# Kernel optimization log

Measured on AMD Instinct MI355X. Metric: run time of the kernel, lower is better.

The kernel has to match this reference:

```python
import jax, jax.numpy as jnp
import numpy as np

TEMPERATURE = 0.07
MARGIN = 0.15
HARD_NEG_RATIO = 0.5


def setup_inputs() -> dict:
    key = jax.random.key(0)
    k1, k2, k3 = jax.random.split(key, 3)
    B, D = 4096, 128
    drug_emb = jax.random.normal(k1, (B, D), dtype=jnp.float32)
    se_emb = jax.random.normal(k2, (B, D), dtype=jnp.float32)
    # labels spread over [0, 5) so that |diff| > 1.0 negatives exist
    labels = jax.random.uniform(k3, (B,), dtype=jnp.float32) * 5.0
    return {"drug_emb": drug_emb, "se_emb": se_emb, "labels": labels}


def _single_branch_loss(z, labels):
    B = z.shape[0]
    # F.normalize(z, dim=-1): divide by norm clamped to eps
    z = z / jnp.maximum(jnp.linalg.norm(z, axis=-1, keepdims=True), 1e-12)
    sim = jnp.matmul(z, z.T) / TEMPERATURE                      # [B, B]
    label_diff = jnp.abs(labels[None, :] - labels[:, None])     # [B, B]
    self_mask = ~jnp.eye(B, dtype=bool)
    pos_weight = jnp.exp(-label_diff / MARGIN) * self_mask      # soft positives
    neg_mask = (label_diff > 1.0) & self_mask

    # k = max(int(mean per-row negative count * ratio), 1), capped at B-1
    mean_negs = jnp.mean(jnp.sum(neg_mask.astype(jnp.float32), axis=1))
    k = jnp.maximum((mean_negs * HARD_NEG_RATIO).astype(jnp.int32), 1)
    k = jnp.minimum(k, B - 1)

    sim_max = jax.lax.stop_gradient(jnp.max(sim, axis=1, keepdims=True))
    logits = sim - sim_max

    # hard-negative top-k per row, as a static-shape rank test (jit-safe)
    neg_sim = jnp.where(neg_mask, sim, -jnp.inf)
    ranks = jnp.argsort(jnp.argsort(-neg_sim, axis=1), axis=1)  # 0 = largest
    hard_neg_mask = (ranks < k) & neg_mask

    any_neg = jnp.any(neg_mask)
    denom_mask = jnp.where(any_neg, hard_neg_mask | (pos_weight > 0.1), self_mask)

    exp_denom = jnp.sum(jnp.exp(logits) * denom_mask, axis=1, keepdims=True) + 1e-8
    log_prob = logits - jnp.log(exp_denom)
    weighted_log_prob = jnp.sum(pos_weight * log_prob, axis=1)
    denom = jnp.maximum(jnp.sum(pos_weight, axis=1), 1e-8)
    return -jnp.mean(weighted_log_prob / denom)


def reference(drug_emb, se_emb, labels):
    loss_drug = _single_branch_loss(drug_emb, labels)
    loss_se = _single_branch_loss(se_emb, labels)
    loss_cross = _single_branch_loss(drug_emb * se_emb, labels)
    return (loss_drug + loss_se + loss_cross) / 3.0
```

## Files before the change

kernel.cpp:

```cpp
#include <hip/hip_runtime.h>
#include <math.h>

#define BB 4096
#define DD 128
#define KLO 0x3E7FFFFFu
#define KHI 0xC1800000u
#define SH0 19
#define NBALLOC 4352

typedef __attribute__((ext_vector_type(8))) short bf16x8;
typedef __attribute__((ext_vector_type(4))) float f32x4;

__device__ __forceinline__ unsigned fkey(float x){
    int b = __float_as_int(x);
    return (unsigned)(b ^ ((b >> 31) | 0x80000000));
}
__device__ __forceinline__ float funkey(unsigned u){
    unsigned b = (u & 0x80000000u) ? (u & 0x7fffffffu) : ~u;
    return __uint_as_float(b);
}

__device__ __forceinline__ float blkSumF(float v, volatile float* sh){
    #pragma unroll
    for (int o = 32; o > 0; o >>= 1) v += __shfl_down(v, o);
    int t = threadIdx.x;
    __syncthreads();
    if ((t & 63) == 0) sh[t >> 6] = v;
    __syncthreads();
    return (sh[0] + sh[1]) + (sh[2] + sh[3]);
}
__device__ __forceinline__ int blkSumI(int v, volatile int* sh){
    #pragma unroll
    for (int o = 32; o > 0; o >>= 1) v += __shfl_down(v, o);
    int t = threadIdx.x;
    __syncthreads();
    if ((t & 63) == 0) sh[t >> 6] = v;
    __syncthreads();
    return (sh[0] + sh[1]) + (sh[2] + sh[3]);
}

__global__ void krn_normalize(const float* __restrict__ drug, const float* __restrict__ se,
                              const float* __restrict__ labels,
                              ushort* __restrict__ Z,
                              float* __restrict__ wp, float* __restrict__ wm){
    int row = blockIdx.x, br = blockIdx.y, t = threadIdx.x;
    float dv = drug[row * DD + t];
    float sv = se[row * DD + t];
    float v = (br == 0) ? dv : ((br == 1) ? sv : dv * sv);
    float sq = v * v;
    #pragma unroll
    for (int o = 32; o > 0; o >>= 1) sq += __shfl_down(sq, o);
    __shared__ float sh[2];
    if ((t & 63) == 0) sh[t >> 6] = sq;
    __syncthreads();
    float nrm = sqrtf(sh[0] + sh[1]);
    float outv = v / fmaxf(nrm, 1e-12f);
    unsigned u = __float_as_uint(outv);
    unsigned r = (u + 0x7FFFu + ((u >> 16) & 1u)) >> 16;
    int col = t ^ ((row & 7) << 3);
    Z[((size_t)br * BB + row) * DD + col] = (ushort)r;
    if (br == 0 && t == 0){
        float l = labels[row];
        wp[row] = __expf(l * (1.0f / 0.15f));
        wm[row] = __expf(l * (-1.0f / 0.15f));
    }
}

__global__ __launch_bounds__(256) void krn_negcount(const float* __restrict__ labels,
                                                    int* __restrict__ ntot){
    __shared__ float lab[BB];
    __shared__ int shi[4];
    int t = threadIdx.x;
    #pragma unroll
    for (int e = 0; e < 4; ++e)
        ((float4*)lab)[t + e * 256] = ((const float4*)labels)[t + e * 256];
    __syncthreads();
    int i0 = blockIdx.x * 16;
    int c = 0;
    for (int ii = 0; ii < 16; ++ii){
        float li = lab[i0 + ii];
        #pragma unroll
        for (int e = 0; e < 16; ++e){
            int j = t + e * 256;
            c += (fabsf(li - lab[j]) > 1.0f) ? 1 : 0;
        }
    }
    int cc = blkSumI(c, shi);
    if (t == 0) atomicAdd(ntot, cc);
}

__global__ void krn_calck(const int* __restrict__ ntot, int* __restrict__ kflags){
    int N = *ntot;
    int k = N >> 13;
    if (k < 1) k = 1;
    if (k > BB - 1) k = BB - 1;
    kflags[0] = k;
    kflags[1] = (N > 0) ? 1 : 0;
}

__device__ __forceinline__ bf16x8 frag_ld(const ushort* base, int row, int e0){
    int e = e0 ^ ((row & 7) << 3);
    return *(const bf16x8*)(base + row * DD + e);
}

__global__ __launch_bounds__(256) void krn_gemm(const ushort* __restrict__ Z,
                                                float* __restrict__ sim, size_t simStride,
                                                int r0){
    __shared__ ushort As[128 * DD];
    __shared__ ushort Bs[128 * DD];
    const ushort* Zb = Z + (size_t)blockIdx.z * (BB * DD);
    float* simz = sim + (size_t)blockIdx.z * simStride;
    int t = threadIdx.x;
    int rowbase = r0 + blockIdx.y * 128;
    int colbase = blockIdx.x * 128;

    {
        const float4* gA = (const float4*)(Zb + (size_t)rowbase * DD);
        const float4* gB = (const float4*)(Zb + (size_t)colbase * DD);
        float4* lA = (float4*)As;
        float4* lB = (float4*)Bs;
        #pragma unroll
        for (int it = 0; it < 8; ++it){
            lA[it * 256 + t] = gA[it * 256 + t];
            lB[it * 256 + t] = gB[it * 256 + t];
        }
    }
    __syncthreads();

    int wid = t >> 6, lane = t & 63;
    int wr = (wid >> 1) * 64, wc = (wid & 1) * 64;
    int fr = lane & 15, fq = lane >> 4;

    f32x4 acc[4][4];
    #pragma unroll
    for (int m = 0; m < 4; ++m)
        #pragma unroll
        for (int n = 0; n < 4; ++n)
            acc[m][n] = (f32x4){0.f, 0.f, 0.f, 0.f};

    #pragma unroll
    for (int ks = 0; ks < 4; ++ks){
        int e0 = ks * 32 + fq * 8;
        bf16x8 a0 = frag_ld(As, wr + 0 * 16 + fr, e0);
        bf16x8 a1 = frag_ld(As, wr + 1 * 16 + fr, e0);
        bf16x8 a2 = frag_ld(As, wr + 2 * 16 + fr, e0);
        bf16x8 a3 = frag_ld(As, wr + 3 * 16 + fr, e0);
        bf16x8 b0 = frag_ld(Bs, wc + 0 * 16 + fr, e0);
        bf16x8 b1 = frag_ld(Bs, wc + 1 * 16 + fr, e0);
        bf16x8 b2 = frag_ld(Bs, wc + 2 * 16 + fr, e0);
        bf16x8 b3 = frag_ld(Bs, wc + 3 * 16 + fr, e0);
        acc[0][0] = __builtin_amdgcn_mfma_f32_16x16x32_bf16(a0, b0, acc[0][0], 0, 0, 0);
        acc[0][1] = __builtin_amdgcn_mfma_f32_16x16x32_bf16(a0, b1, acc[0][1], 0, 0, 0);
        acc[0][2] = __builtin_amdgcn_mfma_f32_16x16x32_bf16(a0, b2, acc[0][2], 0, 0, 0);
        acc[0][3] = __builtin_amdgcn_mfma_f32_16x16x32_bf16(a0, b3, acc[0][3], 0, 0, 0);
        acc[1][0] = __builtin_amdgcn_mfma_f32_16x16x32_bf16(a1, b0, acc[1][0], 0, 0, 0);
        acc[1][1] = __builtin_amdgcn_mfma_f32_16x16x32_bf16(a1, b1, acc[1][1], 0, 0, 0);
        acc[1][2] = __builtin_amdgcn_mfma_f32_16x16x32_bf16(a1, b2, acc[1][2], 0, 0, 0);
        acc[1][3] = __builtin_amdgcn_mfma_f32_16x16x32_bf16(a1, b3, acc[1][3], 0, 0, 0);
        acc[2][0] = __builtin_amdgcn_mfma_f32_16x16x32_bf16(a2, b0, acc[2][0], 0, 0, 0);
        acc[2][1] = __builtin_amdgcn_mfma_f32_16x16x32_bf16(a2, b1, acc[2][1], 0, 0, 0);
        acc[2][2] = __builtin_amdgcn_mfma_f32_16x16x32_bf16(a2, b2, acc[2][2], 0, 0, 0);
        acc[2][3] = __builtin_amdgcn_mfma_f32_16x16x32_bf16(a2, b3, acc[2][3], 0, 0, 0);
        acc[3][0] = __builtin_amdgcn_mfma_f32_16x16x32_bf16(a3, b0, acc[3][0], 0, 0, 0);
        acc[3][1] = __builtin_amdgcn_mfma_f32_16x16x32_bf16(a3, b1, acc[3][1], 0, 0, 0);
        acc[3][2] = __builtin_amdgcn_mfma_f32_16x16x32_bf16(a3, b2, acc[3][2], 0, 0, 0);
        acc[3][3] = __builtin_amdgcn_mfma_f32_16x16x32_bf16(a3, b3, acc[3][3], 0, 0, 0);
    }

    const float invT = 1.0f / 0.07f;
    int srow0 = blockIdx.y * 128 + wr + fq * 4;
    int scol0 = colbase + wc + fr;
    #pragma unroll
    for (int m = 0; m < 4; ++m){
        #pragma unroll
        for (int n = 0; n < 4; ++n){
            f32x4 c = acc[m][n];
            #pragma unroll
            for (int j = 0; j < 4; ++j)
                simz[(size_t)(srow0 + m * 16 + j) * BB + scol0 + n * 16] = c[j] * invT;
        }
    }
}

__global__ __launch_bounds__(256) void krn_stats(const float* __restrict__ sim, size_t simStride,
                                                 const float* __restrict__ labels,
                                                 const float* __restrict__ wp,
                                                 const float* __restrict__ wm,
                                                 const int* __restrict__ kflags,
                                                 float* __restrict__ rowloss, int r0){
    __shared__ int hist[NBALLOC];
    __shared__ int wsum[4];
    __shared__ float redm[4], reda[4], redb[4];
    __shared__ int redn[4];
    __shared__ float redf[4];
    __shared__ unsigned selb[3];
    __shared__ unsigned sel2[2];
    __shared__ int cnt;
    __shared__ unsigned list[64];

    int t = threadIdx.x;
    int bi = blockIdx.y;
    int row = blockIdx.x;
    int i = r0 + row;
    float li = labels[i];
    float sLo = wm[i];
    float sHi = wp[i];

    #pragma unroll
    for (int e = 0; e < 17; ++e) hist[t + e * 256] = 0;
    __syncthreads();

    const float* srow = sim + (size_t)bi * simStride + (size_t)row * BB;
    const float4* sp = (const float4*)srow;
    const float4* lp = (const float4*)labels;
    const float4* pp = (const float4*)wp;
    const float4* mp = (const float4*)wm;

    float s[16];
    unsigned negbits = 0, posbits = 0;
    float m = -INFINITY, pws = 0.f, psim = 0.f;
    int ncnt = 0;

    #pragma unroll
    for (int e = 0; e < 4; ++e){
        float4 sv = sp[t + e * 256];
        float4 lv = lp[t + e * 256];
        float4 pv = pp[t + e * 256];
        float4 mv = mp[t + e * 256];
        float sc[4] = {sv.x, sv.y, sv.z, sv.w};
        float lc[4] = {lv.x, lv.y, lv.z, lv.w};
        float pc[4] = {pv.x, pv.y, pv.z, pv.w};
        float mc[4] = {mv.x, mv.y, mv.z, mv.w};
        #pragma unroll
        for (int c = 0; c < 4; ++c){
            int idx = e * 4 + c;
            float v = sc[c];
            s[idx] = v;
            m = fmaxf(m, v);
            float pw = fminf(sLo * pc[c], sHi * mc[c]);
            pws += pw;
            psim += pw * v;
            float d = fabsf(li - lc[c]);
            if (d > 1.0f){
                negbits |= 1u << idx; ncnt++;
                atomicAdd(&hist[(fkey(v) - KLO) >> SH0], 1);
            } else if (d < 0.34538776f){
                posbits |= 1u << idx;
            }
        }
    }

    #pragma unroll
    for (int o = 32; o > 0; o >>= 1){
        m = fmaxf(m, __shfl_down(m, o));
        pws += __shfl_down(pws, o);
        psim += __shfl_down(psim, o);
        ncnt += __shfl_down(ncnt, o);
    }
    __syncthreads();
    if ((t & 63) == 0){
        int w = t >> 6;
        redm[w] = m; reda[w] = pws; redb[w] = psim; redn[w] = ncnt;
    }
    __syncthreads();
    float M    = fmaxf(fmaxf(redm[0], redm[1]), fmaxf(redm[2], redm[3]));
    float PWS  = (reda[0] + reda[1]) + (reda[2] + reda[3]);
    float PSIM = (redb[0] + redb[1]) + (redb[2] + redb[3]);
    int   NC   = (redn[0] + redn[1]) + (redn[2] + redn[3]);

    int kk = kflags[0], anyneg = kflags[1];
    int mode = anyneg ? ((NC <= kk) ? 1 : 0) : 2;

    unsigned ukth = 0;
    int rfin = 0;
    if (mode == 0){
        unsigned klo = KLO, khi = KHI;
        int sh = SH0;
        int rp = kk;
        bool ready = true;
        while (true){
            if (klo == khi){ ukth = klo; rfin = rp; break; }
            if (!ready){
                #pragma unroll
                for (int e = 0; e < 17; ++e) hist[t + e * 256] = 0;
                __syncthreads();
                #pragma unroll
                for (int idx = 0; idx < 16; ++idx){
                    if (negbits & (1u << idx)){
                        unsigned u = fkey(s[idx]);
                        if (u >= klo && u <= khi)
                            atomicAdd(&hist[(u - klo) >> sh], 1);
                    }
                }
                __syncthreads();
            }
            ready = false;
            int g = 255 - t;
            int base = g * 17;
            int ls = 0;
            #pragma unroll
            for (int e = 0; e < 17; ++e) ls += hist[base + e];
            int v = ls;
            #pragma unroll
            for (int o = 1; o < 64; o <<= 1){
                int u2 = __shfl_up(v, o);
                if ((t & 63) >= o) v += u2;
            }
            if ((t & 63) == 63) wsum[t >> 6] = v;
            __syncthreads();
            int w = t >> 6;
            int pre = (w > 0 ? wsum[0] : 0) + (w > 1 ? wsum[1] : 0) + (w > 2 ? wsum[2] : 0);
            v += pre;
            int aec = v - ls;
            if (aec < rp && rp <= v){
                int cum = aec;
                #pragma unroll
                for (int e = 16; e >= 0; --e){
                    int c = hist[base + e];
                    if (cum < rp && rp <= cum + c){
                        selb[0] = (unsigned)(base + e);
                        selb[1] = (unsigned)cum;
                        selb[2] = (unsigned)c;
                        break;
                    }
                    cum += c;
                }
            }
            __syncthreads();
            unsigned B = selb[0];
            int ae = (int)selb[1];
            int c  = (int)selb[2];
            rp -= ae;
            klo += B << sh;
            unsigned nhi = klo + ((1u << sh) - 1u);
            if (nhi < khi) khi = nhi;
            if (c <= 64){
                if (t == 0) cnt = 0;
                __syncthreads();
                #pragma unroll
                for (int idx = 0; idx < 16; ++idx){
                    if (negbits & (1u << idx)){
                        unsigned u = fkey(s[idx]);
                        if (u >= klo && u <= khi){
                            int p = atomicAdd(&cnt, 1);
                            list[p] = u;
                        }
                    }
                }
                __syncthreads();
                int cc = cnt;
                if (t < cc){
                    unsigned kj = list[t];
                    int g2 = 0, e2 = 0;
                    for (int mm = 0; mm < cc; ++mm){
                        unsigned km = list[mm];
                        g2 += (km > kj) ? 1 : 0;
                        e2 += (km == kj) ? 1 : 0;
                    }
                    if (g2 < rp && rp <= g2 + e2){ sel2[0] = kj; sel2[1] = (unsigned)g2; }
                }
                __syncthreads();
                ukth = sel2[0];
                rfin = rp - (int)sel2[1];
                break;
            }
            {
                unsigned range = khi - klo;
                int bits = 32 - __clz(range);
                sh = (bits > 12) ? (bits - 12) : 0;
            }
            __syncthreads();
        }
    }

    float skth = (mode == 0) ? funkey(ukth) : INFINITY;
    unsigned em = (mode == 2) ? 0xFFFFu : ((mode == 1) ? (negbits | posbits) : posbits);
    float El = 0.f;
    #pragma unroll
    for (int idx = 0; idx < 16; ++idx){
        unsigned bit = 1u << idx;
        bool dm = (em & bit) != 0u;
        if (negbits & bit) dm = dm || (s[idx] > skth);
        if (dm) El += __expf(s[idx] - M);
    }
    float Etot = blkSumF(El, redf);

    if (t == 0){
        if (mode == 0) Etot += (float)rfin * __expf(skth - M);
        float s_self = srow[i];
        float pw_self = sLo * sHi;
        Etot -= __expf(s_self - M);
        float PWSc  = PWS  - pw_self;
        float PSIMc = PSIM - pw_self * s_self;
        float logE = __logf(Etot + 1e-8f);
        float wl = (PSIMc - M * PWSc) - PWSc * logE;
        rowloss[bi * BB + i] = wl / fmaxf(PWSc, 1e-8f);
    }
}

__global__ void krn_final(const float* __restrict__ rowloss, float* __restrict__ out){
    __shared__ float redf[4];
    int t = threadIdx.x;
    float total = 0.f;
    for (int b = 0; b < 3; ++b){
        float ssum = 0.f;
        for (int e = 0; e < 16; ++e) ssum += rowloss[b * BB + t + e * 256];
        float S = blkSumF(ssum, redf);
        total += S * (1.0f / BB);
    }
    if (t == 0) out[0] = -total / 3.0f;
}

extern "C" void kernel_launch(void* const* d_in, const int* in_sizes, int n_in,
                              void* d_out, int out_size, void* d_ws, size_t ws_size,
                              hipStream_t stream){
    const float* drug   = (const float*)d_in[0];
    const float* se     = (const float*)d_in[1];
    const float* labels = (const float*)d_in[2];
    float* out = (float*)d_out;
    char* ws = (char*)d_ws;

    const size_t zbytes = (size_t)3 * BB * DD * sizeof(ushort);
    const size_t tail   = (size_t)(3 + 2) * BB * sizeof(float) + 256;

    int slab = BB;
    while (slab > 128 && zbytes + tail + (size_t)3 * slab * BB * sizeof(float) > ws_size)
        slab >>= 1;
    size_t simStride = (size_t)slab * BB;

    ushort* Z      = (ushort*)ws;
    float* simbuf  = (float*)(ws + zbytes);
    size_t off     = zbytes + (size_t)3 * simStride * sizeof(float);
    float* rowloss = (float*)(ws + off);  off += (size_t)3 * BB * sizeof(float);
    float* wp      = (float*)(ws + off);  off += (size_t)BB * sizeof(float);
    float* wm      = (float*)(ws + off);  off += (size_t)BB * sizeof(float);
    int*   ntot    = (int*)(ws + off);
    int*   kflags  = ntot + 2;

    hipMemsetAsync(ntot, 0, 2 * sizeof(int), stream);
    krn_normalize<<<dim3(BB, 3), 128, 0, stream>>>(drug, se, labels, Z, wp, wm);
    krn_negcount<<<256, 256, 0, stream>>>(labels, ntot);
    krn_calck<<<1, 1, 0, stream>>>(ntot, kflags);

    int nslab = BB / slab;
    for (int s2 = 0; s2 < nslab; ++s2){
        krn_gemm<<<dim3(BB / 128, slab / 128, 3), 256, 0, stream>>>(Z, simbuf, simStride, s2 * slab);
        krn_stats<<<dim3(slab, 3), 256, 0, stream>>>(simbuf, simStride, labels, wp, wm,
                                                     kflags, rowloss, s2 * slab);
    }
    krn_final<<<1, 256, 0, stream>>>(rowloss, out);
}
```

Before: 185.7 us.

## Move positive-weight sums into label pass and GEMM epilogue

```diff
diff --git a/kernel.cpp b/kernel.cpp
--- a/kernel.cpp
+++ b/kernel.cpp
@@ -28,6 +28,15 @@
     if ((t & 63) == 0) sh[t >> 6] = v;
     __syncthreads();
     return (sh[0] + sh[1]) + (sh[2] + sh[3]);
+}
+__device__ __forceinline__ float blkMaxF(float v, volatile float* sh){
+    #pragma unroll
+    for (int o = 32; o > 0; o >>= 1) v = fmaxf(v, __shfl_down(v, o));
+    int t = threadIdx.x;
+    __syncthreads();
+    if ((t & 63) == 0) sh[t >> 6] = v;
+    __syncthreads();
+    return fmaxf(fmaxf(sh[0], sh[1]), fmaxf(sh[2], sh[3]));
 }
 __device__ __forceinline__ int blkSumI(int v, volatile int* sh){
     #pragma unroll
@@ -66,27 +75,39 @@
     }
 }
 
-__global__ __launch_bounds__(256) void krn_negcount(const float* __restrict__ labels,
-                                                    int* __restrict__ ntot){
+__global__ __launch_bounds__(256) void krn_labelstats(const float* __restrict__ labels,
+                                                      int* __restrict__ NC,
+                                                      float* __restrict__ PWS,
+                                                      int* __restrict__ ntot){
     __shared__ float lab[BB];
     __shared__ int shi[4];
+    __shared__ float shf[4];
     int t = threadIdx.x;
     #pragma unroll
     for (int e = 0; e < 4; ++e)
         ((float4*)lab)[t + e * 256] = ((const float4*)labels)[t + e * 256];
     __syncthreads();
     int i0 = blockIdx.x * 16;
-    int c = 0;
+    int ctot = 0;
     for (int ii = 0; ii < 16; ++ii){
         float li = lab[i0 + ii];
+        int c = 0;
+        float pws = 0.f;
         #pragma unroll
         for (int e = 0; e < 16; ++e){
-            int j = t + e * 256;
-            c += (fabsf(li - lab[j]) > 1.0f) ? 1 : 0;
-        }
-    }
-    int cc = blkSumI(c, shi);
-    if (t == 0) atomicAdd(ntot, cc);
+            float d = fabsf(li - lab[t + e * 256]);
+            c += (d > 1.0f) ? 1 : 0;
+            pws += __expf(d * (-1.0f / 0.15f));
+        }
+        int C = blkSumI(c, shi);
+        float P = blkSumF(pws, shf);
+        if (t == 0){
+            NC[i0 + ii] = C;
+            PWS[i0 + ii] = P - 1.0f;
+            ctot += C;
+        }
+    }
+    if (t == 0) atomicAdd(ntot, ctot);
 }
 
 __global__ void krn_calck(const int* __restrict__ ntot, int* __restrict__ kflags){
@@ -105,9 +126,13 @@
 
 __global__ __launch_bounds__(256) void krn_gemm(const ushort* __restrict__ Z,
                                                 float* __restrict__ sim, size_t simStride,
+                                                const float* __restrict__ wp,
+                                                const float* __restrict__ wm,
+                                                float* __restrict__ psim,
                                                 int r0){
     __shared__ ushort As[128 * DD];
     __shared__ ushort Bs[128 * DD];
+    __shared__ float wpA[128], wmA[128], wpB[128], wmB[128];
     const ushort* Zb = Z + (size_t)blockIdx.z * (BB * DD);
     float* simz = sim + (size_t)blockIdx.z * simStride;
     int t = threadIdx.x;
@@ -123,6 +148,14 @@
         for (int it = 0; it < 8; ++it){
             lA[it * 256 + t] = gA[it * 256 + t];
             lB[it * 256 + t] = gB[it * 256 + t];
+        }
+        if (t < 128){
+            wpA[t] = wp[rowbase + t];
+            wmA[t] = wm[rowbase + t];
+        } else {
+            int u2 = t - 128;
+            wpB[u2] = wp[colbase + u2];
+            wmB[u2] = wm[colbase + u2];
         }
     }
     __syncthreads();
@@ -180,18 +213,47 @@
                 simz[(size_t)(srow0 + m * 16 + j) * BB + scol0 + n * 16] = c[j] * invT;
         }
     }
+
+    float* psimz = psim + (size_t)blockIdx.z * BB;
+    float wpc[4], wmc[4];
+    #pragma unroll
+    for (int n = 0; n < 4; ++n){
+        int cl = wc + n * 16 + fr;
+        wpc[n] = wpB[cl];
+        wmc[n] = wmB[cl];
+    }
+    #pragma unroll
+    for (int m = 0; m < 4; ++m){
+        #pragma unroll
+        for (int j = 0; j < 4; ++j){
+            int rl = wr + m * 16 + fq * 4 + j;
+            float wpr = wpA[rl], wmr = wmA[rl];
+            float p = 0.f;
+            #pragma unroll
+            for (int n = 0; n < 4; ++n){
+                float svv = acc[m][n][j] * invT;
+                float pw = fminf(wpr * wmc[n], wmr * wpc[n]);
+                p = fmaf(pw, svv, p);
+            }
+            #pragma unroll
+            for (int o = 1; o < 16; o <<= 1) p += __shfl_xor(p, o);
+            if (fr == 0)
+                atomicAdd(&psimz[rowbase + rl], p);
+        }
+    }
 }
 
 __global__ __launch_bounds__(256) void krn_stats(const float* __restrict__ sim, size_t simStride,
                                                  const float* __restrict__ labels,
                                                  const float* __restrict__ wp,
                                                  const float* __restrict__ wm,
+                                                 const int* __restrict__ NC,
+                                                 const float* __restrict__ PWSg,
+                                                 const float* __restrict__ psimg,
                                                  const int* __restrict__ kflags,
                                                  float* __restrict__ rowloss, int r0){
     __shared__ int hist[NBALLOC];
     __shared__ int wsum[4];
-    __shared__ float redm[4], reda[4], redb[4];
-    __shared__ int redn[4];
     __shared__ float redf[4];
     __shared__ unsigned selb[3];
     __shared__ unsigned sel2[2];
@@ -203,8 +265,6 @@
     int row = blockIdx.x;
     int i = r0 + row;
     float li = labels[i];
-    float sLo = wm[i];
-    float sHi = wp[i];
 
     #pragma unroll
     for (int e = 0; e < 17; ++e) hist[t + e * 256] = 0;
@@ -213,36 +273,26 @@
     const float* srow = sim + (size_t)bi * simStride + (size_t)row * BB;
     const float4* sp = (const float4*)srow;
     const float4* lp = (const float4*)labels;
-    const float4* pp = (const float4*)wp;
-    const float4* mp = (const float4*)wm;
 
     float s[16];
     unsigned negbits = 0, posbits = 0;
-    float m = -INFINITY, pws = 0.f, psim = 0.f;
-    int ncnt = 0;
+    float m = -INFINITY;
 
     #pragma unroll
     for (int e = 0; e < 4; ++e){
         float4 sv = sp[t + e * 256];
         float4 lv = lp[t + e * 256];
-        float4 pv = pp[t + e * 256];
-        float4 mv = mp[t + e * 256];
         float sc[4] = {sv.x, sv.y, sv.z, sv.w};
         float lc[4] = {lv.x, lv.y, lv.z, lv.w};
-        float pc[4] = {pv.x, pv.y, pv.z, pv.w};
-        float mc[4] = {mv.x, mv.y, mv.z, mv.w};
         #pragma unroll
         for (int c = 0; c < 4; ++c){
             int idx = e * 4 + c;
             float v = sc[c];
             s[idx] = v;
             m = fmaxf(m, v);
-            float pw = fminf(sLo * pc[c], sHi * mc[c]);
-            pws += pw;
-            psim += pw * v;
             float d = fabsf(li - lc[c]);
             if (d > 1.0f){
-                negbits |= 1u << idx; ncnt++;
+                negbits |= 1u << idx;
                 atomicAdd(&hist[(fkey(v) - KLO) >> SH0], 1);
             } else if (d < 0.34538776f){
                 posbits |= 1u << idx;
@@ -250,26 +300,11 @@
         }
     }
 
-    #pragma unroll
-    for (int o = 32; o > 0; o >>= 1){
-        m = fmaxf(m, __shfl_down(m, o));
-        pws += __shfl_down(pws, o);
-        psim += __shfl_down(psim, o);
-        ncnt += __shfl_down(ncnt, o);
-    }
-    __syncthreads();
-    if ((t & 63) == 0){
-        int w = t >> 6;
-        redm[w] = m; reda[w] = pws; redb[w] = psim; redn[w] = ncnt;
-    }
-    __syncthreads();
-    float M    = fmaxf(fmaxf(redm[0], redm[1]), fmaxf(redm[2], redm[3]));
-    float PWS  = (reda[0] + reda[1]) + (reda[2] + reda[3]);
-    float PSIM = (redb[0] + redb[1]) + (redb[2] + redb[3]);
-    int   NC   = (redn[0] + redn[1]) + (redn[2] + redn[3]);
+    float M = blkMaxF(m, redf);
 
     int kk = kflags[0], anyneg = kflags[1];
-    int mode = anyneg ? ((NC <= kk) ? 1 : 0) : 2;
+    int NCv = NC[i];
+    int mode = anyneg ? ((NCv <= kk) ? 1 : 0) : 2;
 
     unsigned ukth = 0;
     int rfin = 0;
@@ -388,10 +423,10 @@
     if (t == 0){
         if (mode == 0) Etot += (float)rfin * __expf(skth - M);
         float s_self = srow[i];
-        float pw_self = sLo * sHi;
         Etot -= __expf(s_self - M);
-        float PWSc  = PWS  - pw_self;
-        float PSIMc = PSIM - pw_self * s_self;
+        float pwii = wp[i] * wm[i];
+        float PWSc  = PWSg[i];
+        float PSIMc = psimg[bi * BB + i] - s_self * pwii;
         float logE = __logf(Etot + 1e-8f);
         float wl = (PSIMc - M * PWSc) - PWSc * logE;
         rowloss[bi * BB + i] = wl / fmaxf(PWSc, 1e-8f);
@@ -421,7 +456,7 @@
     char* ws = (char*)d_ws;
 
     const size_t zbytes = (size_t)3 * BB * DD * sizeof(ushort);
-    const size_t tail   = (size_t)(3 + 2) * BB * sizeof(float) + 256;
+    const size_t tail   = (size_t)(3 + 2 + 3 + 1 + 1) * BB * sizeof(float) + 256;
 
     int slab = BB;
     while (slab > 128 && zbytes + tail + (size_t)3 * slab * BB * sizeof(float) > ws_size)
@@ -434,19 +469,24 @@
     float* rowloss = (float*)(ws + off);  off += (size_t)3 * BB * sizeof(float);
     float* wp      = (float*)(ws + off);  off += (size_t)BB * sizeof(float);
     float* wm      = (float*)(ws + off);  off += (size_t)BB * sizeof(float);
+    float* psim    = (float*)(ws + off);  off += (size_t)3 * BB * sizeof(float);
+    float* PWSb    = (float*)(ws + off);  off += (size_t)BB * sizeof(float);
+    int*   NCb     = (int*)(ws + off);    off += (size_t)BB * sizeof(int);
     int*   ntot    = (int*)(ws + off);
     int*   kflags  = ntot + 2;
 
     hipMemsetAsync(ntot, 0, 2 * sizeof(int), stream);
+    hipMemsetAsync(psim, 0, (size_t)3 * BB * sizeof(float), stream);
     krn_normalize<<<dim3(BB, 3), 128, 0, stream>>>(drug, se, labels, Z, wp, wm);
-    krn_negcount<<<256, 256, 0, stream>>>(labels, ntot);
+    krn_labelstats<<<256, 256, 0, stream>>>(labels, NCb, PWSb, ntot);
     krn_calck<<<1, 1, 0, stream>>>(ntot, kflags);
 
     int nslab = BB / slab;
     for (int s2 = 0; s2 < nslab; ++s2){
-        krn_gemm<<<dim3(BB / 128, slab / 128, 3), 256, 0, stream>>>(Z, simbuf, simStride, s2 * slab);
+        krn_gemm<<<dim3(BB / 128, slab / 128, 3), 256, 0, stream>>>(Z, simbuf, simStride,
+                                                                    wp, wm, psim, s2 * slab);
         krn_stats<<<dim3(slab, 3), 256, 0, stream>>>(simbuf, simStride, labels, wp, wm,
-                                                     kflags, rowloss, s2 * slab);
+                                                     NCb, PWSb, psim, kflags, rowloss, s2 * slab);
     }
     krn_final<<<1, 256, 0, stream>>>(rowloss, out);
 }
```

Result: slower. 216.6 us (+16.7%).

## Store similarity matrix in fp16 and precompute per-row label statistics

Applied to the files above, without the earlier changes.

```diff
diff --git a/kernel.cpp b/kernel.cpp
--- a/kernel.cpp
+++ b/kernel.cpp
@@ -10,6 +10,7 @@
 
 typedef __attribute__((ext_vector_type(8))) short bf16x8;
 typedef __attribute__((ext_vector_type(4))) float f32x4;
+typedef __attribute__((ext_vector_type(4))) _Float16 f16x4;
 
 __device__ __forceinline__ unsigned fkey(float x){
     int b = __float_as_int(x);
@@ -40,9 +41,7 @@
 }
 
 __global__ void krn_normalize(const float* __restrict__ drug, const float* __restrict__ se,
-                              const float* __restrict__ labels,
-                              ushort* __restrict__ Z,
-                              float* __restrict__ wp, float* __restrict__ wm){
+                              ushort* __restrict__ Z){
     int row = blockIdx.x, br = blockIdx.y, t = threadIdx.x;
     float dv = drug[row * DD + t];
     float sv = se[row * DD + t];
@@ -59,34 +58,41 @@
     unsigned r = (u + 0x7FFFu + ((u >> 16) & 1u)) >> 16;
     int col = t ^ ((row & 7) << 3);
     Z[((size_t)br * BB + row) * DD + col] = (ushort)r;
-    if (br == 0 && t == 0){
-        float l = labels[row];
-        wp[row] = __expf(l * (1.0f / 0.15f));
-        wm[row] = __expf(l * (-1.0f / 0.15f));
-    }
-}
-
-__global__ __launch_bounds__(256) void krn_negcount(const float* __restrict__ labels,
-                                                    int* __restrict__ ntot){
+}
+
+__global__ __launch_bounds__(256) void krn_labelstats(const float* __restrict__ labels,
+                                                      int* __restrict__ NC,
+                                                      float* __restrict__ PWS,
+                                                      int* __restrict__ ntot){
     __shared__ float lab[BB];
     __shared__ int shi[4];
+    __shared__ float shf[4];
     int t = threadIdx.x;
     #pragma unroll
     for (int e = 0; e < 4; ++e)
         ((float4*)lab)[t + e * 256] = ((const float4*)labels)[t + e * 256];
     __syncthreads();
     int i0 = blockIdx.x * 16;
-    int c = 0;
+    int ctot = 0;
     for (int ii = 0; ii < 16; ++ii){
         float li = lab[i0 + ii];
+        int c = 0;
+        float pws = 0.f;
         #pragma unroll
         for (int e = 0; e < 16; ++e){
-            int j = t + e * 256;
-            c += (fabsf(li - lab[j]) > 1.0f) ? 1 : 0;
-        }
-    }
-    int cc = blkSumI(c, shi);
-    if (t == 0) atomicAdd(ntot, cc);
+            float d = fabsf(li - lab[t + e * 256]);
+            c += (d > 1.0f) ? 1 : 0;
+            pws += __expf(d * (-1.0f / 0.15f));
+        }
+        int C = blkSumI(c, shi);
+        float P = blkSumF(pws, shf);
+        if (t == 0){
+            NC[i0 + ii] = C;
+            PWS[i0 + ii] = P - 1.0f;
+            ctot += C;
+        }
+    }
+    if (t == 0) atomicAdd(ntot, ctot);
 }
 
 __global__ void krn_calck(const int* __restrict__ ntot, int* __restrict__ kflags){
@@ -104,12 +110,12 @@
 }
 
 __global__ __launch_bounds__(256) void krn_gemm(const ushort* __restrict__ Z,
-                                                float* __restrict__ sim, size_t simStride,
+                                                _Float16* __restrict__ sim, size_t simStride,
                                                 int r0){
     __shared__ ushort As[128 * DD];
     __shared__ ushort Bs[128 * DD];
     const ushort* Zb = Z + (size_t)blockIdx.z * (BB * DD);
-    float* simz = sim + (size_t)blockIdx.z * simStride;
+    _Float16* simz = sim + (size_t)blockIdx.z * simStride;
     int t = threadIdx.x;
     int rowbase = r0 + blockIdx.y * 128;
     int colbase = blockIdx.x * 128;
@@ -177,72 +183,60 @@
             f32x4 c = acc[m][n];
             #pragma unroll
             for (int j = 0; j < 4; ++j)
-                simz[(size_t)(srow0 + m * 16 + j) * BB + scol0 + n * 16] = c[j] * invT;
-        }
-    }
-}
-
-__global__ __launch_bounds__(256) void krn_stats(const float* __restrict__ sim, size_t simStride,
+                simz[(size_t)(srow0 + m * 16 + j) * BB + scol0 + n * 16] = (_Float16)(c[j] * invT);
+        }
+    }
+}
+
+__global__ __launch_bounds__(256) void krn_stats(const _Float16* __restrict__ sim, size_t simStride,
                                                  const float* __restrict__ labels,
-                                                 const float* __restrict__ wp,
-                                                 const float* __restrict__ wm,
+                                                 const int* __restrict__ NC,
+                                                 const float* __restrict__ PWSg,
                                                  const int* __restrict__ kflags,
                                                  float* __restrict__ rowloss, int r0){
     __shared__ int hist[NBALLOC];
     __shared__ int wsum[4];
-    __shared__ float redm[4], reda[4], redb[4];
-    __shared__ int redn[4];
+    __shared__ float redm[4], redb[4];
     __shared__ float redf[4];
     __shared__ unsigned selb[3];
     __shared__ unsigned sel2[2];
     __shared__ int cnt;
-    __shared__ unsigned list[64];
+    __shared__ unsigned list[96];
 
     int t = threadIdx.x;
     int bi = blockIdx.y;
     int row = blockIdx.x;
     int i = r0 + row;
     float li = labels[i];
-    float sLo = wm[i];
-    float sHi = wp[i];
 
     #pragma unroll
     for (int e = 0; e < 17; ++e) hist[t + e * 256] = 0;
     __syncthreads();
 
-    const float* srow = sim + (size_t)bi * simStride + (size_t)row * BB;
-    const float4* sp = (const float4*)srow;
+    const _Float16* srow = sim + (size_t)bi * simStride + (size_t)row * BB;
+    const f16x4* sp = (const f16x4*)srow;
     const float4* lp = (const float4*)labels;
-    const float4* pp = (const float4*)wp;
-    const float4* mp = (const float4*)wm;
 
     float s[16];
     unsigned negbits = 0, posbits = 0;
-    float m = -INFINITY, pws = 0.f, psim = 0.f;
-    int ncnt = 0;
+    float m = -INFINITY, psim = 0.f;
 
     #pragma unroll
     for (int e = 0; e < 4; ++e){
-        float4 sv = sp[t + e * 256];
+        f16x4 hv = sp[t + e * 256];
         float4 lv = lp[t + e * 256];
-        float4 pv = pp[t + e * 256];
-        float4 mv = mp[t + e * 256];
-        float sc[4] = {sv.x, sv.y, sv.z, sv.w};
         float lc[4] = {lv.x, lv.y, lv.z, lv.w};
-        float pc[4] = {pv.x, pv.y, pv.z, pv.w};
-        float mc[4] = {mv.x, mv.y, mv.z, mv.w};
         #pragma unroll
         for (int c = 0; c < 4; ++c){
             int idx = e * 4 + c;
-            float v = sc[c];
+            float v = (float)hv[c];
             s[idx] = v;
             m = fmaxf(m, v);
-            float pw = fminf(sLo * pc[c], sHi * mc[c]);
-            pws += pw;
-            psim += pw * v;
             float d = fabsf(li - lc[c]);
+            float pw = __expf(d * (-1.0f / 0.15f));
+            psim = fmaf(pw, v, psim);
             if (d > 1.0f){
-                negbits |= 1u << idx; ncnt++;
+                negbits |= 1u << idx;
                 atomicAdd(&hist[(fkey(v) - KLO) >> SH0], 1);
             } else if (d < 0.34538776f){
                 posbits |= 1u << idx;
@@ -253,23 +247,20 @@
     #pragma unroll
     for (int o = 32; o > 0; o >>= 1){
         m = fmaxf(m, __shfl_down(m, o));
-        pws += __shfl_down(pws, o);
         psim += __shfl_down(psim, o);
-        ncnt += __shfl_down(ncnt, o);
     }
     __syncthreads();
     if ((t & 63) == 0){
         int w = t >> 6;
-        redm[w] = m; reda[w] = pws; redb[w] = psim; redn[w] = ncnt;
+        redm[w] = m; redb[w] = psim;
     }
     __syncthreads();
     float M    = fmaxf(fmaxf(redm[0], redm[1]), fmaxf(redm[2], redm[3]));
-    float PWS  = (reda[0] + reda[1]) + (reda[2] + reda[3]);
     float PSIM = (redb[0] + redb[1]) + (redb[2] + redb[3]);
-    int   NC   = (redn[0] + redn[1]) + (redn[2] + redn[3]);
 
     int kk = kflags[0], anyneg = kflags[1];
-    int mode = anyneg ? ((NC <= kk) ? 1 : 0) : 2;
+    int NCv = NC[i];
+    int mode = anyneg ? ((NCv <= kk) ? 1 : 0) : 2;
 
     unsigned ukth = 0;
     int rfin = 0;
@@ -334,7 +325,7 @@
             klo += B << sh;
             unsigned nhi = klo + ((1u << sh) - 1u);
             if (nhi < khi) khi = nhi;
-            if (c <= 64){
+            if (c <= 96){
                 if (t == 0) cnt = 0;
                 __syncthreads();
                 #pragma unroll
@@ -387,11 +378,10 @@
 
     if (t == 0){
         if (mode == 0) Etot += (float)rfin * __expf(skth - M);
-        float s_self = srow[i];
-        float pw_self = sLo * sHi;
+        float s_self = (float)srow[i];
         Etot -= __expf(s_self - M);
-        float PWSc  = PWS  - pw_self;
-        float PSIMc = PSIM - pw_self * s_self;
+        float PWSc  = PWSg[i];
+        float PSIMc = PSIM - s_self;
         float logE = __logf(Etot + 1e-8f);
         float wl = (PSIMc - M * PWSc) - PWSc * logE;
         rowloss[bi * BB + i] = wl / fmaxf(PWSc, 1e-8f);
@@ -421,32 +411,32 @@
     char* ws = (char*)d_ws;
 
     const size_t zbytes = (size_t)3 * BB * DD * sizeof(ushort);
-    const size_t tail   = (size_t)(3 + 2) * BB * sizeof(float) + 256;
+    const size_t tail   = (size_t)(3 + 1 + 1) * BB * sizeof(float) + 256;
 
     int slab = BB;
-    while (slab > 128 && zbytes + tail + (size_t)3 * slab * BB * sizeof(float) > ws_size)
+    while (slab > 128 && zbytes + tail + (size_t)3 * slab * BB * sizeof(_Float16) > ws_size)
         slab >>= 1;
     size_t simStride = (size_t)slab * BB;
 
-    ushort* Z      = (ushort*)ws;
-    float* simbuf  = (float*)(ws + zbytes);
-    size_t off     = zbytes + (size_t)3 * simStride * sizeof(float);
+    ushort* Z          = (ushort*)ws;
+    _Float16* simbuf   = (_Float16*)(ws + zbytes);
+    size_t off         = zbytes + (size_t)3 * simStride * sizeof(_Float16);
     float* rowloss = (float*)(ws + off);  off += (size_t)3 * BB * sizeof(float);
-    float* wp      = (float*)(ws + off);  off += (size_t)BB * sizeof(float);
-    float* wm      = (float*)(ws + off);  off += (size_t)BB * sizeof(float);
+    float* PWSb    = (float*)(ws + off);  off += (size_t)BB * sizeof(float);
+    int*   NCb     = (int*)(ws + off);    off += (size_t)BB * sizeof(int);
     int*   ntot    = (int*)(ws + off);
     int*   kflags  = ntot + 2;
 
     hipMemsetAsync(ntot, 0, 2 * sizeof(int), stream);
-    krn_normalize<<<dim3(BB, 3), 128, 0, stream>>>(drug, se, labels, Z, wp, wm);
-    krn_negcount<<<256, 256, 0, stream>>>(labels, ntot);
+    krn_normalize<<<dim3(BB, 3), 128, 0, stream>>>(drug, se, Z);
+    krn_labelstats<<<256, 256, 0, stream>>>(labels, NCb, PWSb, ntot);
     krn_calck<<<1, 1, 0, stream>>>(ntot, kflags);
 
     int nslab = BB / slab;
     for (int s2 = 0; s2 < nslab; ++s2){
         krn_gemm<<<dim3(BB / 128, slab / 128, 3), 256, 0, stream>>>(Z, simbuf, simStride, s2 * slab);
-        krn_stats<<<dim3(slab, 3), 256, 0, stream>>>(simbuf, simStride, labels, wp, wm,
-                                                     kflags, rowloss, s2 * slab);
+        krn_stats<<<dim3(slab, 3), 256, 0, stream>>>(simbuf, simStride, labels,
+                                                     NCb, PWSb, kflags, rowloss, s2 * slab);
     }
     krn_final<<<1, 256, 0, stream>>>(rowloss, out);
 }
```

New measurement: 191.6 us. 1.03x slower.
